# Kernel tuning notes

Hardware: AMD Instinct MI355X
Metric: run time of the kernel (lower is better)

The kernel has to match this reference:

```python
import jax, jax.numpy as jnp
import numpy as np

B, NP, L, C, NA = 16, 512, 20, 3, 50
RATIO = 0.8
K = int(np.ceil(RATIO * NP))  # 410 nodes kept per graph
N = B * NP
E = 6 * N
NF, EF = 13, 4
EPS = 1e-5


def _graph_norm(x, w, b, ms):
    # PyG GraphNorm called WITHOUT batch in the source -> single global graph
    mean = x.mean(0)
    out = x - ms * mean
    var = (out * out).mean(0)
    return w * out / jnp.sqrt(var + EPS) + b


def _forward(x, pan_w, lin1_w, lin1_b, norm1_w, norm1_b, norm1_ms,
             pool_p, pool_beta, gat_wl, gat_bl, gat_wr, gat_br, gat_att, gat_bias,
             norm2_w, norm2_b, norm2_ms,
             val1_w, val1_b, val2_w, val2_b, val3_w, val3_b,
             adv1_w, adv1_b, adv2_w, adv2_b, adv3_w, adv3_b,
             edge_index, current_node_ids, action_mask):
    src, dst = edge_index[0], edge_index[1]
    # PANConv builds SparseTensor(row=edge_index[1], col=edge_index[0]) -> row = target
    A = jnp.zeros((B, NP, NP), x.dtype).at[dst // NP, dst % NP, src % NP].set(1.0)
    eyeB = jnp.broadcast_to(jnp.eye(NP, dtype=x.dtype), A.shape)

    # panentropy: M = sum_{i=0..L} w_i * A^i  (dense per graph)
    def step(carry, wi):
        tmp, acc = carry
        tmp = tmp @ A
        return (tmp, acc + wi * tmp), None
    (_, M), _ = jax.lax.scan(step, (eyeB, pan_w[0] * eyeB), pan_w[1:])
    deg = M.sum(-1)                                   # row sums
    dis = jnp.where(deg > 0, 1.0 / jnp.sqrt(deg), 0.0)
    Mn = dis[:, :, None] * M * dis[:, None, :]        # D^-1/2 M D^-1/2

    # conv1: propagate (Mn @ x) then Linear
    x3 = x.reshape(B, NP, NF)
    h = jnp.einsum('bij,bjf->bif', Mn, x3) @ lin1_w + lin1_b   # [B,NP,C]
    x1 = jax.nn.relu(_graph_norm(h.reshape(N, C), norm1_w, norm1_b, norm1_ms))  # [N,C]
    h = x1.reshape(B, NP, C)

    # PANPooling: score = tanh(b0 * <x,p> + b1 * colsum(Mn)); keep top K per graph
    score = jnp.tanh(pool_beta[0] * (h * pool_p).sum(-1) + pool_beta[1] * Mn.sum(-2))
    vals, idx = jax.lax.top_k(score, K)                        # [B,K]
    xp = jnp.take_along_axis(h, idx[:, :, None], axis=1) * vals[..., None]
    Mg = jax.vmap(lambda m, i: m[i][:, i])(Mn, idx)            # filtered adjacency [B,K,K]
    mask = (jnp.swapaxes(Mg, 1, 2) != 0) | jnp.eye(K, dtype=bool)  # mask[b,i,j]: edge j->i (+self loops)

    # GATv2Conv, heads=1, eval mode (no dropout), edge_attr not passed in source
    xl = xp @ gat_wl + gat_bl
    xr = xp @ gat_wr + gat_br
    e = jax.nn.leaky_relu(xr[:, :, None, :] + xl[:, None, :, :], 0.2)  # [B,i,j,C]
    logits = jnp.where(mask, jnp.einsum('bijc,c->bij', e, gat_att), -1e9)
    alpha = jax.nn.softmax(logits, axis=-1)
    g = jnp.einsum('bij,bjc->bic', alpha, xl) + gat_bias

    g = jax.nn.relu(_graph_norm(g.reshape(B * K, C), norm2_w, norm2_b, norm2_ms)).reshape(B, K, C)
    gp = g.sum(1)                                              # global_add_pool [B,C]

    # source uses POOLED bincount cumsum offsets to index the pre-pool arrays (faithful)
    gidx = current_node_ids + jnp.arange(B, dtype=current_node_ids.dtype) * K
    feat = jnp.concatenate([x[gidx], x1[gidx], gp], axis=1)    # [B,19]

    a = jax.nn.relu(feat @ adv1_w + adv1_b)
    a = jax.nn.relu(a @ adv2_w + adv2_b)
    a = a @ adv3_w + adv3_b
    v = jax.nn.relu(feat @ val1_w + val1_b)
    v = jax.nn.relu(v @ val2_w + val2_b)
    v = v @ val3_w + val3_b
    q = v + (a - a.mean(1, keepdims=True))
    return jnp.where(action_mask == 0, -1e8, q)


def setup_inputs() -> dict:
    key = jax.random.key(0)
    ks = list(jax.random.split(key, 40))
    nk = lambda: ks.pop()
    # within-graph random edges so the PyG-style batch structure is valid
    g = jax.random.randint(nk(), (E,), 0, B)
    u = jax.random.randint(nk(), (E,), 0, NP)
    v = jax.random.randint(nk(), (E,), 0, NP)
    edge_index = jnp.stack([g * NP + u, g * NP + v]).astype(jnp.int32)

    def lin(k, i, o):
        k1, k2 = jax.random.split(k)
        return (jax.random.normal(k1, (i, o), jnp.float32) / np.sqrt(i),
                jax.random.normal(k2, (o,), jnp.float32) * 0.01)

    lin1_w, lin1_b = lin(nk(), NF, C)
    gat_wl, gat_bl = lin(nk(), C, C)
    gat_wr, gat_br = lin(nk(), C, C)
    val1_w, val1_b = lin(nk(), 19, 10)
    val2_w, val2_b = lin(nk(), 10, 5)
    val3_w, val3_b = lin(nk(), 5, 1)
    adv1_w, adv1_b = lin(nk(), 19, 10)
    adv2_w, adv2_b = lin(nk(), 10, 5)
    adv3_w, adv3_b = lin(nk(), 5, NA)
    return dict(
        x=jax.random.normal(nk(), (N, NF), jnp.float32),
        edge_index=edge_index,
        edge_attr=jax.random.normal(nk(), (E, EF), jnp.float32),
        batch=jnp.arange(N, dtype=jnp.int32) // NP,
        current_node_ids=jax.random.randint(nk(), (B,), 0, NP),
        action_mask=jax.random.randint(nk(), (B, NA), 0, 2),
        pan_w=jax.random.uniform(nk(), (L + 1,), jnp.float32) * 0.5,
        lin1_w=lin1_w, lin1_b=lin1_b,
        norm1_w=jnp.ones(C), norm1_b=jnp.zeros(C), norm1_ms=jnp.ones(C),
        pool_p=jax.random.normal(nk(), (C,), jnp.float32),
        pool_beta=jnp.array([0.5, 0.5], jnp.float32),
        gat_wl=gat_wl, gat_bl=gat_bl, gat_wr=gat_wr, gat_br=gat_br,
        gat_att=jax.random.normal(nk(), (C,), jnp.float32),
        gat_bias=jax.random.normal(nk(), (C,), jnp.float32) * 0.01,
        norm2_w=jnp.ones(C), norm2_b=jnp.zeros(C), norm2_ms=jnp.ones(C),
        val1_w=val1_w, val1_b=val1_b, val2_w=val2_w, val2_b=val2_b,
        val3_w=val3_w, val3_b=val3_b,
        adv1_w=adv1_w, adv1_b=adv1_b, adv2_w=adv2_w, adv2_b=adv2_b,
        adv3_w=adv3_w, adv3_b=adv3_b,
    )


def reference(x, edge_index, edge_attr, batch, current_node_ids, action_mask,
              pan_w, lin1_w, lin1_b, norm1_w, norm1_b, norm1_ms,
              pool_p, pool_beta, gat_wl, gat_bl, gat_wr, gat_br, gat_att, gat_bias,
              norm2_w, norm2_b, norm2_ms,
              val1_w, val1_b, val2_w, val2_b, val3_w, val3_b,
              adv1_w, adv1_b, adv2_w, adv2_b, adv3_w, adv3_b):
    del edge_attr, batch  # received by the torch forward but never consumed
    return _forward(x, pan_w, lin1_w, lin1_b, norm1_w, norm1_b, norm1_ms,
                    pool_p, pool_beta, gat_wl, gat_bl, gat_wr, gat_br, gat_att, gat_bias,
                    norm2_w, norm2_b, norm2_ms,
                    val1_w, val1_b, val2_w, val2_b, val3_w, val3_b,
                    adv1_w, adv1_b, adv2_w, adv2_b, adv3_w, adv3_b,
                    edge_index, current_node_ids, action_mask)
```

## Files before the change

kernel.cpp:

```cpp
#include <hip/hip_runtime.h>
#include <hip/hip_bf16.h>
#include <stdint.h>
#include <math.h>

#define BB   16
#define NPn  512
#define LLp  20
#define NAa  50
#define KKk  410
#define NNt  (BB * NPn)
#define EEe  (6 * NNt)
#define NFf  13
#define KPAD 416
#define KP2  448
#define EPSf 1e-5f
#define QCLMP 1e6f
#define MAXD 28
#define PADR 512

__device__ __forceinline__ float r16_sane(float v) {
    if (!(v == v)) return 0.0f;
    return fminf(fmaxf(v, -1e15f), 1e15f);
}

__global__ __launch_bounds__(512) void r16_build(
    const int* __restrict__ ei,
    unsigned short* __restrict__ csrF, unsigned short* __restrict__ csrT)
{
    __shared__ uint32_t fw[NPn * 16];
    __shared__ uint32_t tr[NPn * 16];
    const int b = blockIdx.x, t = threadIdx.x;
#pragma unroll
    for (int w = 0; w < 16; ++w) { fw[t * 16 + w] = 0u; tr[t * 16 + w] = 0u; }
    __syncthreads();
    for (int e = t; e < EEe; e += 512) {
        const int src = ei[e], dst = ei[EEe + e];
        if ((dst >> 9) == b)
            atomicOr(&fw[(dst & 511) * 16 + ((src & 511) >> 5)], 1u << (src & 31));
        if ((src >> 9) == b)
            atomicOr(&tr[(src & 511) * 16 + ((dst & 511) >> 5)], 1u << (dst & 31));
    }
    __syncthreads();
    const int node = b * 512 + t;
    {
        int cnt = 0;
        for (int w = 0; w < 16; ++w) {
            uint32_t bits = fw[t * 16 + w];
            while (bits) {
                const int u = (w << 5) + __ffs(bits) - 1;
                bits &= bits - 1;
                if (cnt < MAXD) csrF[(size_t)cnt * 8192 + node] = (unsigned short)u;
                ++cnt;
            }
        }
        for (int j = cnt; j < MAXD; ++j) csrF[(size_t)j * 8192 + node] = PADR;
    }
    {
        int cnt = 0;
        for (int w = 0; w < 16; ++w) {
            uint32_t bits = tr[t * 16 + w];
            while (bits) {
                const int u = (w << 5) + __ffs(bits) - 1;
                bits &= bits - 1;
                if (cnt < MAXD) csrT[(size_t)cnt * 8192 + node] = (unsigned short)u;
                ++cnt;
            }
        }
        for (int j = cnt; j < MAXD; ++j) csrT[(size_t)j * 8192 + node] = PADR;
    }
}

__global__ __launch_bounds__(512) void r16_mid(
    const float* __restrict__ x,
    const unsigned short* __restrict__ csrF,
    const unsigned short* __restrict__ csrT,
    const float* __restrict__ panw,
    const float* __restrict__ l1w, const float* __restrict__ l1b,
    float* __restrict__ h_raw, float* __restrict__ colsum,
    uint32_t* __restrict__ Rb)
{
    __shared__ __align__(16) uint32_t sbuf[1047];
    float* pa  = (float*)sbuf;
    float* pb  = (float*)(sbuf + 513);
    float* wsh = (float*)(sbuf + 1026);
    const int b = blockIdx.x, y = blockIdx.y, t = threadIdx.x;
    const int node = b * 512 + t;

    if (y < 4) {
        const int c = y;
        int iF[MAXD];
#pragma unroll
        for (int j = 0; j < MAXD; ++j) iF[j] = (int)csrF[(size_t)j * 8192 + node];
        if (t < 21) wsh[t] = panw[t];

        pa[t] = 1.0f;
        if (t == 0) { pa[512] = 0.0f; pb[512] = 0.0f; }
        __syncthreads();
        float dacc = wsh[0];
        {
            float* rp = pa; float* rn = pb;
            for (int i = 1; i <= LLp; ++i) {
                float tv[MAXD];
#pragma unroll
                for (int j = 0; j < MAXD; ++j) tv[j] = rp[iF[j]];
                float s = 0.0f;
#pragma unroll
                for (int j = 0; j < MAXD; ++j) s += tv[j];
                rn[t] = s;
                dacc += wsh[i] * s;
                __syncthreads();
                float* tp = rp; rp = rn; rn = tp;
            }
        }
        const float d0 = (dacc > 0.0f) ? 1.0f / sqrtf(dacc) : 0.0f;

        int idx[MAXD];
        if (c == 3) {
#pragma unroll
            for (int j = 0; j < MAXD; ++j) idx[j] = (int)csrT[(size_t)j * 8192 + node];
        } else {
#pragma unroll
            for (int j = 0; j < MAXD; ++j) idx[j] = iF[j];
        }
        float seed;
        if (c < 3) {
            float xw = 0.0f;
            const float* xr = x + (size_t)node * NFf;
            for (int f = 0; f < NFf; ++f) xw += xr[f] * l1w[f * 3 + c];
            seed = d0 * xw;
        } else {
            seed = d0;
        }
        pa[t] = seed;
        if (t == 0) { pa[512] = 0.0f; pb[512] = 0.0f; }
        __syncthreads();
        float acc = wsh[0] * seed;
        {
            float* rp = pa; float* rn = pb;
            for (int i = 1; i <= LLp; ++i) {
                float tv[MAXD];
#pragma unroll
                for (int j = 0; j < MAXD; ++j) tv[j] = rp[idx[j]];
                float s = 0.0f;
#pragma unroll
                for (int j = 0; j < MAXD; ++j) s += tv[j];
                rn[t] = s;
                acc += wsh[i] * s;
                __syncthreads();
                float* tp = rp; rp = rn; rn = tp;
            }
        }
        if (c < 3) h_raw[(size_t)node * 3 + c] = r16_sane(d0 * acc + l1b[c]);
        else       colsum[node] = r16_sane(d0 * acc);
    } else {
        const int q = y - 4;
        int iF[MAXD];
#pragma unroll
        for (int j = 0; j < MAXD; ++j) iF[j] = (int)csrF[(size_t)j * 8192 + node];
        uint32_t* R1 = sbuf;
        uint32_t* R2 = sbuf + 513;
        R1[t] = ((t >> 5) == q) ? (1u << (t & 31)) : 0u;
        if (t == 0) { R1[512] = 0u; R2[512] = 0u; }
        __syncthreads();
        uint32_t* Rp = R1; uint32_t* Rn = R2;
        for (int i = 0; i < LLp; ++i) {
            uint32_t tv[MAXD];
#pragma unroll
            for (int j = 0; j < MAXD; ++j) tv[j] = Rp[iF[j]];
            uint32_t r = Rp[t];
#pragma unroll
            for (int j = 0; j < MAXD; ++j) r |= tv[j];
            Rn[t] = r;
            __syncthreads();
            uint32_t* tp = Rp; Rp = Rn; Rn = tp;
        }
        Rb[(size_t)node * 16 + q] = Rp[t];
    }
}

__global__ __launch_bounds__(512) void r16_poolgat(
    const float* __restrict__ h_raw,
    const float* __restrict__ colsum,
    const uint32_t* __restrict__ Rb,
    const float* n1w, const float* n1b, const float* n1ms,
    const float* poolp, const float* poolb,
    const float* gwl, const float* gbl,
    const float* gwr, const float* gbr,
    const float* gatt, const float* gbias,
    float* __restrict__ x1,
    float* __restrict__ g_raw)
{
    __shared__ __align__(16) uint32_t pg[10744];
    float* sc   = (float*)pg;
    float* mv   = (float*)(pg + 512);
    float* wred = (float*)(pg + 520);
    float* xpS  = (float*)(pg + 568);
    int*   kidx = (int*)(pg + 1816);
    float* xlS  = (float*)(pg + 2232);
    uint32_t* RT = pg + 3576;
    const int b = blockIdx.x, y = blockIdx.y, t = threadIdx.x;
    const int lane = t & 63, wv = t >> 6;
    const float inv_n = 1.0f / (float)NNt;

    float hv0[16], hv1[16], hv2[16];
    float p0 = 0.0f, p1 = 0.0f, p2 = 0.0f;
#pragma unroll
    for (int k = 0; k < 16; ++k) {
        const float* hr = h_raw + (size_t)(k * 512 + t) * 3;
        hv0[k] = hr[0]; hv1[k] = hr[1]; hv2[k] = hr[2];
        p0 += hv0[k]; p1 += hv1[k]; p2 += hv2[k];
    }
#pragma unroll
    for (int off = 32; off; off >>= 1) {
        p0 += __shfl_xor(p0, off); p1 += __shfl_xor(p1, off); p2 += __shfl_xor(p2, off);
    }
    if (lane == 0) { wred[wv * 3 + 0] = p0; wred[wv * 3 + 1] = p1; wred[wv * 3 + 2] = p2; }
    __syncthreads();
    if (t < 3) {
        float s = 0.0f;
        for (int w = 0; w < 8; ++w) s += wred[w * 3 + t];
        mv[t] = s * inv_n;
    }
    __syncthreads();
    const float mm0 = n1ms[0] * mv[0], mm1 = n1ms[1] * mv[1], mm2 = n1ms[2] * mv[2];
    float q0 = 0.0f, q1 = 0.0f, q2 = 0.0f;
#pragma unroll
    for (int k = 0; k < 16; ++k) {
        const float d0 = hv0[k] - mm0, d1 = hv1[k] - mm1, d2 = hv2[k] - mm2;
        q0 += d0 * d0; q1 += d1 * d1; q2 += d2 * d2;
    }
#pragma unroll
    for (int off = 32; off; off >>= 1) {
        q0 += __shfl_xor(q0, off); q1 += __shfl_xor(q1, off); q2 += __shfl_xor(q2, off);
    }
    if (lane == 0) { wred[wv * 3 + 0] = q0; wred[wv * 3 + 1] = q1; wred[wv * 3 + 2] = q2; }
    __syncthreads();
    if (t < 3) {
        float s = 0.0f;
        for (int w = 0; w < 8; ++w) s += wred[w * 3 + t];
        mv[3 + t] = s * inv_n;
    }
    __syncthreads();

    const float mmv[3] = { mm0, mm1, mm2 };
    float xv[3];
#pragma unroll
    for (int c = 0; c < 3; ++c) {
        const float iv = 1.0f / sqrtf(fmaxf(mv[3 + c], 0.0f) + EPSf);
        const float o  = h_raw[(size_t)(b * NPn + t) * 3 + c] - mmv[c];
        const float tt = n1w[c] * o * iv + n1b[c];
        xv[c] = fmaxf(tt, 0.0f);
        if (y == 0) x1[(size_t)(b * NPn + t) * 3 + c] = xv[c];
    }
    float s = poolb[0] * (xv[0] * poolp[0] + xv[1] * poolp[1] + xv[2] * poolp[2])
            + poolb[1] * colsum[b * NPn + t];
    s = tanhf(s);
    if (!(s == s)) s = 0.0f;
    sc[t] = s;
    __syncthreads();
    int cnt = 0;
    for (int u = 0; u < NPn; ++u) {
        const float su = sc[u];
        cnt += ((su > s) || (su == s && u < t)) ? 1 : 0;
    }
    if (cnt < KKk) {
        kidx[cnt] = t;
        xpS[cnt * 3 + 0] = xv[0] * s;
        xpS[cnt * 3 + 1] = xv[1] * s;
        xpS[cnt * 3 + 2] = xv[2] * s;
    }
    __syncthreads();

    float Wl[9], Wr[9];
#pragma unroll
    for (int i2 = 0; i2 < 9; ++i2) { Wl[i2] = gwl[i2]; Wr[i2] = gwr[i2]; }
    const float Bl0 = gbl[0], Bl1 = gbl[1], Bl2 = gbl[2];
    const float Br0 = gbr[0], Br1 = gbr[1], Br2 = gbr[2];
    const float At0 = gatt[0], At1 = gatt[1], At2 = gatt[2];
    const float Gb0 = gbias[0], Gb1 = gbias[1], Gb2 = gbias[2];
    if (t < KP2) {
        const int j = t;
        if (j < KKk) {
            const float c0 = xpS[j * 3 + 0];
            const float c1 = xpS[j * 3 + 1];
            const float c2 = xpS[j * 3 + 2];
            xlS[j * 3 + 0] = c0 * Wl[0] + c1 * Wl[3] + c2 * Wl[6] + Bl0;
            xlS[j * 3 + 1] = c0 * Wl[1] + c1 * Wl[4] + c2 * Wl[7] + Bl1;
            xlS[j * 3 + 2] = c0 * Wl[2] + c1 * Wl[5] + c2 * Wl[8] + Bl2;
            const uint32_t* rr = Rb + (size_t)(b * NPn + kidx[j]) * 16;
#pragma unroll
            for (int w = 0; w < 16; ++w) RT[w * KP2 + j] = rr[w];
        } else {
            xlS[j * 3 + 0] = 0.0f; xlS[j * 3 + 1] = 0.0f; xlS[j * 3 + 2] = 0.0f;
#pragma unroll
            for (int w = 0; w < 16; ++w) RT[w * KP2 + j] = 0u;
        }
    }
    __syncthreads();

    const int wid = y * 8 + wv;
    for (int i = wid; i < KKk; i += 64) {
        const float c0 = xpS[i * 3 + 0];
        const float c1 = xpS[i * 3 + 1];
        const float c2 = xpS[i * 3 + 2];
        const float xr0 = c0 * Wr[0] + c1 * Wr[3] + c2 * Wr[6] + Br0;
        const float xr1 = c0 * Wr[1] + c1 * Wr[4] + c2 * Wr[7] + Br1;
        const float xr2 = c0 * Wr[2] + c1 * Wr[5] + c2 * Wr[8] + Br2;
        const int bi = kidx[i];
        const uint32_t mbit = 1u << (bi & 31);
        const uint32_t* Rw = &RT[(bi >> 5) * KP2];
        float mx = -3e38f, lsum = 0.0f, b0 = 0.0f, b1 = 0.0f, b2 = 0.0f;
#pragma unroll
        for (int it = 0; it < 7; ++it) {
            const int j = lane + it * 64;
            const uint32_t rw = Rw[j];
            const float xl0 = xlS[j * 3 + 0];
            const float xl1 = xlS[j * 3 + 1];
            const float xl2 = xlS[j * 3 + 2];
            const bool valid = (rw & mbit) || (j == i);
            float e0 = xr0 + xl0; e0 = e0 > 0.0f ? e0 : 0.2f * e0;
            float e1 = xr1 + xl1; e1 = e1 > 0.0f ? e1 : 0.2f * e1;
            float e2 = xr2 + xl2; e2 = e2 > 0.0f ? e2 : 0.2f * e2;
            const float sv = At0 * e0 + At1 * e1 + At2 * e2;
            if (valid) {
                if (sv > mx) {
                    const float r = __expf(mx - sv);
                    lsum *= r; b0 *= r; b1 *= r; b2 *= r;
                    mx = sv;
                }
                const float pj = __expf(sv - mx);
                lsum += pj;
                b0 += pj * xl0; b1 += pj * xl1; b2 += pj * xl2;
            }
        }
#pragma unroll
        for (int off = 32; off; off >>= 1) {
            const float mo = __shfl_xor(mx, off);
            const float lo = __shfl_xor(lsum, off);
            const float d0 = __shfl_xor(b0, off);
            const float d1 = __shfl_xor(b1, off);
            const float d2 = __shfl_xor(b2, off);
            const float M  = fmaxf(mx, mo);
            const float ea = __expf(mx - M), eb = __expf(mo - M);
            lsum = lsum * ea + lo * eb;
            b0 = b0 * ea + d0 * eb;
            b1 = b1 * ea + d1 * eb;
            b2 = b2 * ea + d2 * eb;
            mx = M;
        }
        if (lane == 0) {
            const float rl = 1.0f / fmaxf(lsum, 1e-30f);
            g_raw[(size_t)(b * KPAD + i) * 3 + 0] = r16_sane(b0 * rl + Gb0);
            g_raw[(size_t)(b * KPAD + i) * 3 + 1] = r16_sane(b1 * rl + Gb1);
            g_raw[(size_t)(b * KPAD + i) * 3 + 2] = r16_sane(b2 * rl + Gb2);
        }
    }
}

__global__ __launch_bounds__(512) void r16_head(
    const float* __restrict__ g_raw,
    const float* __restrict__ x1,
    const float* __restrict__ x,
    const int* __restrict__ cnid,
    const int* __restrict__ amask,
    const float* n2w, const float* n2b, const float* n2ms,
    const float* v1w, const float* v1b,
    const float* v2w, const float* v2b,
    const float* v3w, const float* v3b,
    const float* a1w, const float* a1b,
    const float* a2w, const float* a2b,
    const float* a3w, const float* a3b,
    float* __restrict__ out)
{
    __shared__ float wred[24];
    __shared__ float mv[6];
    __shared__ float gp[3];
    __shared__ float feat[19];
    __shared__ float h1a[10], h1v[10], h2a[5], h2v[5];
    __shared__ float a3[50];
    __shared__ float vout_s, amean_s;
    const int b = blockIdx.x, t = threadIdx.x;
    const int lane = t & 63, wv = t >> 6;
    const float denom = 1.0f / (float)(BB * KKk);

    float gv0[13], gv1[13], gv2[13];
    float p0 = 0.0f, p1 = 0.0f, p2 = 0.0f;
#pragma unroll
    for (int k = 0; k < 13; ++k) {
        const int r = k * 512 + t;
        float q0 = 0.0f, q1 = 0.0f, q2 = 0.0f;
        if (r < BB * KKk) {
            const int bq = r / KKk, iq = r - bq * KKk;
            const float* gr = g_raw + (size_t)(bq * KPAD + iq) * 3;
            q0 = gr[0]; q1 = gr[1]; q2 = gr[2];
        }
        gv0[k] = q0; gv1[k] = q1; gv2[k] = q2;
        p0 += q0; p1 += q1; p2 += q2;
    }
#pragma unroll
    for (int off = 32; off; off >>= 1) {
        p0 += __shfl_xor(p0, off); p1 += __shfl_xor(p1, off); p2 += __shfl_xor(p2, off);
    }
    if (lane == 0) { wred[wv * 3 + 0] = p0; wred[wv * 3 + 1] = p1; wred[wv * 3 + 2] = p2; }
    __syncthreads();
    if (t < 3) {
        float s = 0.0f;
        for (int w = 0; w < 8; ++w) s += wred[w * 3 + t];
        mv[t] = s * denom;
    }
    __syncthreads();
    const float mm0 = n2ms[0] * mv[0], mm1 = n2ms[1] * mv[1], mm2 = n2ms[2] * mv[2];
    float q0a = 0.0f, q1a = 0.0f, q2a = 0.0f;
#pragma unroll
    for (int k = 0; k < 13; ++k) {
        const int r = k * 512 + t;
        if (r < BB * KKk) {
            const float d0 = gv0[k] - mm0, d1 = gv1[k] - mm1, d2 = gv2[k] - mm2;
            q0a += d0 * d0; q1a += d1 * d1; q2a += d2 * d2;
        }
    }
#pragma unroll
    for (int off = 32; off; off >>= 1) {
        q0a += __shfl_xor(q0a, off); q1a += __shfl_xor(q1a, off); q2a += __shfl_xor(q2a, off);
    }
    if (lane == 0) { wred[wv * 3 + 0] = q0a; wred[wv * 3 + 1] = q1a; wred[wv * 3 + 2] = q2a; }
    __syncthreads();
    if (t < 3) {
        float s = 0.0f;
        for (int w = 0; w < 8; ++w) s += wred[w * 3 + t];
        mv[3 + t] = s * denom;
    }
    __syncthreads();

    const float mmv[3] = { mm0, mm1, mm2 };
    float s3[3] = { 0.0f, 0.0f, 0.0f };
    if (t < KKk) {
        const size_t r = (size_t)(b * KPAD + t) * 3;
#pragma unroll
        for (int c = 0; c < 3; ++c) {
            const float iv = 1.0f / sqrtf(fmaxf(mv[3 + c], 0.0f) + EPSf);
            s3[c] = fmaxf((g_raw[r + c] - mmv[c]) * iv * n2w[c] + n2b[c], 0.0f);
        }
    }
    float g0 = s3[0], g1 = s3[1], g2 = s3[2];
#pragma unroll
    for (int off = 32; off; off >>= 1) {
        g0 += __shfl_xor(g0, off); g1 += __shfl_xor(g1, off); g2 += __shfl_xor(g2, off);
    }
    if (lane == 0) { wred[wv * 3 + 0] = g0; wred[wv * 3 + 1] = g1; wred[wv * 3 + 2] = g2; }
    __syncthreads();
    if (t < 3) {
        float s = 0.0f;
        for (int w = 0; w < 8; ++w) s += wred[w * 3 + t];
        gp[t] = s;
    }
    __syncthreads();

    if (t < 19) {
        const int gidx = cnid[b] + b * KKk;
        float fv;
        if (t < 13)      fv = x[(size_t)gidx * NFf + t];
        else if (t < 16) fv = x1[(size_t)gidx * 3 + (t - 13)];
        else             fv = gp[t - 16];
        feat[t] = fv;
    }
    __syncthreads();

    if (t < 10) {
        float s = a1b[t];
        for (int f = 0; f < 19; ++f) s += feat[f] * a1w[f * 10 + t];
        h1a[t] = fmaxf(s, 0.0f);
    } else if (t >= 64 && t < 74) {
        const int j = t - 64;
        float s = v1b[j];
        for (int f = 0; f < 19; ++f) s += feat[f] * v1w[f * 10 + j];
        h1v[j] = fmaxf(s, 0.0f);
    }
    __syncthreads();
    if (t < 5) {
        float s = a2b[t];
        for (int k = 0; k < 10; ++k) s += h1a[k] * a2w[k * 5 + t];
        h2a[t] = fmaxf(s, 0.0f);
    } else if (t >= 64 && t < 69) {
        const int j = t - 64;
        float s = v2b[j];
        for (int k = 0; k < 10; ++k) s += h1v[k] * v2w[k * 5 + j];
        h2v[j] = fmaxf(s, 0.0f);
    }
    __syncthreads();
    if (t < 50) {
        float s = a3b[t];
        for (int k = 0; k < 5; ++k) s += h2a[k] * a3w[k * 50 + t];
        a3[t] = s;
    } else if (t == 64) {
        float s = v3b[0];
        for (int k = 0; k < 5; ++k) s += h2v[k] * v3w[k];
        vout_s = s;
    }
    __syncthreads();
    if (t == 0) {
        float s = 0.0f;
        for (int k = 0; k < 50; ++k) s += a3[k];
        amean_s = s * (1.0f / 50.0f);
    }
    __syncthreads();
    if (t < 50) {
        float q = vout_s + a3[t] - amean_s;
        if (!(q == q)) q = 0.0f;
        q = fminf(fmaxf(q, -QCLMP), QCLMP);
        out[b * NAa + t] = (amask[b * NAa + t] == 0) ? -1e8f : q;
    }
}

extern "C" void kernel_launch(void* const* d_in, const int* in_sizes, int n_in,
                              void* d_out, int out_size, void* d_ws, size_t ws_size,
                              hipStream_t stream) {
    (void)in_sizes; (void)n_in; (void)out_size;
    const float* x     = (const float*)d_in[0];
    const int* ei      = (const int*)d_in[1];
    const int* cnid    = (const int*)d_in[4];
    const int* amask   = (const int*)d_in[5];
    const float* panw  = (const float*)d_in[6];
    const float* l1w   = (const float*)d_in[7];
    const float* l1b   = (const float*)d_in[8];
    const float* n1w   = (const float*)d_in[9];
    const float* n1b   = (const float*)d_in[10];
    const float* n1ms  = (const float*)d_in[11];
    const float* poolp = (const float*)d_in[12];
    const float* poolb = (const float*)d_in[13];
    const float* gwl   = (const float*)d_in[14];
    const float* gbl   = (const float*)d_in[15];
    const float* gwr   = (const float*)d_in[16];
    const float* gbr   = (const float*)d_in[17];
    const float* gatt  = (const float*)d_in[18];
    const float* gbias = (const float*)d_in[19];
    const float* n2w   = (const float*)d_in[20];
    const float* n2b   = (const float*)d_in[21];
    const float* n2ms  = (const float*)d_in[22];
    const float* v1w   = (const float*)d_in[23];
    const float* v1b   = (const float*)d_in[24];
    const float* v2w   = (const float*)d_in[25];
    const float* v2b   = (const float*)d_in[26];
    const float* v3w   = (const float*)d_in[27];
    const float* v3b   = (const float*)d_in[28];
    const float* a1w   = (const float*)d_in[29];
    const float* a1b   = (const float*)d_in[30];
    const float* a2w   = (const float*)d_in[31];
    const float* a2b   = (const float*)d_in[32];
    const float* a3w   = (const float*)d_in[33];
    const float* a3b   = (const float*)d_in[34];
    float* out         = (float*)d_out;

    uint8_t* wsb = (uint8_t*)d_ws;
    uint32_t* Rb   = (uint32_t*)wsb;
    unsigned short* csrF = (unsigned short*)(wsb + 524288);
    unsigned short* csrT = csrF + (size_t)MAXD * 8192;
    float* h_raw  = (float*)(csrT + (size_t)MAXD * 8192);
    float* x1     = h_raw + (size_t)NNt * 3;
    float* colsum = x1 + (size_t)NNt * 3;
    float* g_raw  = colsum + NNt;
    const size_t needed = 524288 + 2 * (size_t)MAXD * 8192 * 2 +
                          ((size_t)(2 * NNt * 3 + NNt + BB * KPAD * 3)) * 4;
    if (ws_size < needed) return;

    r16_build<<<dim3(16), dim3(512), 0, stream>>>(ei, csrF, csrT);
    r16_mid<<<dim3(16, 20), dim3(512), 0, stream>>>(x, csrF, csrT, panw, l1w, l1b,
                                                    h_raw, colsum, Rb);
    r16_poolgat<<<dim3(16, 8), dim3(512), 0, stream>>>(h_raw, colsum, Rb,
                                                       n1w, n1b, n1ms, poolp, poolb,
                                                       gwl, gbl, gwr, gbr, gatt, gbias,
                                                       x1, g_raw);
    r16_head<<<dim3(16), dim3(512), 0, stream>>>(g_raw, x1, x, cnid, amask,
                                                 n2w, n2b, n2ms, v1w, v1b, v2w, v2b, v3w, v3b,
                                                 a1w, a1b, a2w, a2b, a3w, a3b, out);
}
```

Measured before the change: 247.6 us.

## Split graph build into global atomic scatter and parallel CSR extraction kernels

Replaces the 16-block build kernel, in which every block scanned all edges and filtered by graph, with a memset plus a scatter kernel that launches one thread per edge and ORs adjacency bits into global bitmaps. A separate kernel with one thread per node and direction then extracts the padded CSR lists. This removes the redundant 16x edge scan and the low occupancy of 16 blocks, at the cost of global atomics, an extra memset and two more launches.

```diff
diff --git a/kernel.cpp b/kernel.cpp
--- a/kernel.cpp
+++ b/kernel.cpp
@@ -18,59 +18,46 @@
 #define MAXD 28
 #define PADR 512
 
-__device__ __forceinline__ float r16_sane(float v) {
+__device__ __forceinline__ float r17_sane(float v) {
     if (!(v == v)) return 0.0f;
     return fminf(fmaxf(v, -1e15f), 1e15f);
 }
 
-__global__ __launch_bounds__(512) void r16_build(
+__global__ __launch_bounds__(256) void r17_scatter(
     const int* __restrict__ ei,
+    uint32_t* __restrict__ fwdb, uint32_t* __restrict__ trsb)
+{
+    const int e = blockIdx.x * 256 + threadIdx.x;
+    if (e < EEe) {
+        const int src = ei[e], dst = ei[EEe + e];
+        atomicOr(&fwdb[(size_t)dst * 16 + ((src & 511) >> 5)], 1u << (src & 31));
+        atomicOr(&trsb[(size_t)src * 16 + ((dst & 511) >> 5)], 1u << (dst & 31));
+    }
+}
+
+__global__ __launch_bounds__(256) void r17_extract(
+    const uint32_t* __restrict__ fwdb, const uint32_t* __restrict__ trsb,
     unsigned short* __restrict__ csrF, unsigned short* __restrict__ csrT)
 {
-    __shared__ uint32_t fw[NPn * 16];
-    __shared__ uint32_t tr[NPn * 16];
-    const int b = blockIdx.x, t = threadIdx.x;
-#pragma unroll
-    for (int w = 0; w < 16; ++w) { fw[t * 16 + w] = 0u; tr[t * 16 + w] = 0u; }
-    __syncthreads();
-    for (int e = t; e < EEe; e += 512) {
-        const int src = ei[e], dst = ei[EEe + e];
-        if ((dst >> 9) == b)
-            atomicOr(&fw[(dst & 511) * 16 + ((src & 511) >> 5)], 1u << (src & 31));
-        if ((src >> 9) == b)
-            atomicOr(&tr[(src & 511) * 16 + ((dst & 511) >> 5)], 1u << (dst & 31));
-    }
-    __syncthreads();
-    const int node = b * 512 + t;
-    {
-        int cnt = 0;
-        for (int w = 0; w < 16; ++w) {
-            uint32_t bits = fw[t * 16 + w];
-            while (bits) {
-                const int u = (w << 5) + __ffs(bits) - 1;
-                bits &= bits - 1;
-                if (cnt < MAXD) csrF[(size_t)cnt * 8192 + node] = (unsigned short)u;
-                ++cnt;
-            }
-        }
-        for (int j = cnt; j < MAXD; ++j) csrF[(size_t)j * 8192 + node] = PADR;
-    }
-    {
-        int cnt = 0;
-        for (int w = 0; w < 16; ++w) {
-            uint32_t bits = tr[t * 16 + w];
-            while (bits) {
-                const int u = (w << 5) + __ffs(bits) - 1;
-                bits &= bits - 1;
-                if (cnt < MAXD) csrT[(size_t)cnt * 8192 + node] = (unsigned short)u;
-                ++cnt;
-            }
-        }
-        for (int j = cnt; j < MAXD; ++j) csrT[(size_t)j * 8192 + node] = PADR;
-    }
-}
-
-__global__ __launch_bounds__(512) void r16_mid(
+    const int t = blockIdx.x * 256 + threadIdx.x;
+    const int node = t & 8191;
+    const uint32_t* bs = (t < 8192) ? (fwdb + (size_t)node * 16)
+                                    : (trsb + (size_t)node * 16);
+    unsigned short* cs = (t < 8192) ? csrF : csrT;
+    int cnt = 0;
+    for (int w = 0; w < 16; ++w) {
+        uint32_t bits = bs[w];
+        while (bits) {
+            const int u = (w << 5) + __ffs(bits) - 1;
+            bits &= bits - 1;
+            if (cnt < MAXD) cs[(size_t)cnt * 8192 + node] = (unsigned short)u;
+            ++cnt;
+        }
+    }
+    for (int j = cnt; j < MAXD; ++j) cs[(size_t)j * 8192 + node] = PADR;
+}
+
+__global__ __launch_bounds__(512) void r17_mid(
     const float* __restrict__ x,
     const unsigned short* __restrict__ csrF,
     const unsigned short* __restrict__ csrT,
@@ -150,8 +137,8 @@
                 float* tp = rp; rp = rn; rn = tp;
             }
         }
-        if (c < 3) h_raw[(size_t)node * 3 + c] = r16_sane(d0 * acc + l1b[c]);
-        else       colsum[node] = r16_sane(d0 * acc);
+        if (c < 3) h_raw[(size_t)node * 3 + c] = r17_sane(d0 * acc + l1b[c]);
+        else       colsum[node] = r17_sane(d0 * acc);
     } else {
         const int q = y - 4;
         int iF[MAXD];
@@ -178,7 +165,7 @@
     }
 }
 
-__global__ __launch_bounds__(512) void r16_poolgat(
+__global__ __launch_bounds__(512) void r17_poolgat(
     const float* __restrict__ h_raw,
     const float* __restrict__ colsum,
     const uint32_t* __restrict__ Rb,
@@ -350,14 +337,14 @@
         }
         if (lane == 0) {
             const float rl = 1.0f / fmaxf(lsum, 1e-30f);
-            g_raw[(size_t)(b * KPAD + i) * 3 + 0] = r16_sane(b0 * rl + Gb0);
-            g_raw[(size_t)(b * KPAD + i) * 3 + 1] = r16_sane(b1 * rl + Gb1);
-            g_raw[(size_t)(b * KPAD + i) * 3 + 2] = r16_sane(b2 * rl + Gb2);
-        }
-    }
-}
-
-__global__ __launch_bounds__(512) void r16_head(
+            g_raw[(size_t)(b * KPAD + i) * 3 + 0] = r17_sane(b0 * rl + Gb0);
+            g_raw[(size_t)(b * KPAD + i) * 3 + 1] = r17_sane(b1 * rl + Gb1);
+            g_raw[(size_t)(b * KPAD + i) * 3 + 2] = r17_sane(b2 * rl + Gb2);
+        }
+    }
+}
+
+__global__ __launch_bounds__(512) void r17_head(
     const float* __restrict__ g_raw,
     const float* __restrict__ x1,
     const float* __restrict__ x,
@@ -552,25 +539,29 @@
     float* out         = (float*)d_out;
 
     uint8_t* wsb = (uint8_t*)d_ws;
-    uint32_t* Rb   = (uint32_t*)wsb;
-    unsigned short* csrF = (unsigned short*)(wsb + 524288);
+    uint32_t* fwdb = (uint32_t*)wsb;
+    uint32_t* trsb = (uint32_t*)(wsb + 524288);
+    uint32_t* Rb   = (uint32_t*)(wsb + 1048576);
+    unsigned short* csrF = (unsigned short*)(wsb + 1572864);
     unsigned short* csrT = csrF + (size_t)MAXD * 8192;
     float* h_raw  = (float*)(csrT + (size_t)MAXD * 8192);
     float* x1     = h_raw + (size_t)NNt * 3;
     float* colsum = x1 + (size_t)NNt * 3;
     float* g_raw  = colsum + NNt;
-    const size_t needed = 524288 + 2 * (size_t)MAXD * 8192 * 2 +
+    const size_t needed = 1572864 + 2 * (size_t)MAXD * 8192 * 2 +
                           ((size_t)(2 * NNt * 3 + NNt + BB * KPAD * 3)) * 4;
     if (ws_size < needed) return;
 
-    r16_build<<<dim3(16), dim3(512), 0, stream>>>(ei, csrF, csrT);
-    r16_mid<<<dim3(16, 20), dim3(512), 0, stream>>>(x, csrF, csrT, panw, l1w, l1b,
+    hipMemsetAsync(fwdb, 0, 1048576, stream);
+    r17_scatter<<<dim3((EEe + 255) / 256), dim3(256), 0, stream>>>(ei, fwdb, trsb);
+    r17_extract<<<dim3(64), dim3(256), 0, stream>>>(fwdb, trsb, csrF, csrT);
+    r17_mid<<<dim3(16, 20), dim3(512), 0, stream>>>(x, csrF, csrT, panw, l1w, l1b,
                                                     h_raw, colsum, Rb);
-    r16_poolgat<<<dim3(16, 8), dim3(512), 0, stream>>>(h_raw, colsum, Rb,
+    r17_poolgat<<<dim3(16, 8), dim3(512), 0, stream>>>(h_raw, colsum, Rb,
                                                        n1w, n1b, n1ms, poolp, poolb,
                                                        gwl, gbl, gwr, gbr, gatt, gbias,
                                                        x1, g_raw);
-    r16_head<<<dim3(16), dim3(512), 0, stream>>>(g_raw, x1, x, cnid, amask,
+    r17_head<<<dim3(16), dim3(512), 0, stream>>>(g_raw, x1, x, cnid, amask,
                                                  n2w, n2b, n2ms, v1w, v1b, v2w, v2b, v3w, v3b,
                                                  a1w, a1b, a2w, a2b, a3w, a3b, out);
 }
```

New measurement: 208.7 us. 1.19x faster.
